# Performance work log

Hardware: AMD Instinct MI355X
Metric: run time of the kernel (lower is better)

## Reference

```python
import jax, jax.numpy as jnp
import numpy as np

B, O, N = 8, 100, 4096
TOK_D, D, K, H = 2048, 256, 128, 8
DH = D // H
LN_EPS = 1e-5


def _ln(x, g, b):
    m = x.mean(-1, keepdims=True)
    v = ((x - m) ** 2).mean(-1, keepdims=True)
    return (x - m) * jax.lax.rsqrt(v + LN_EPS) * g + b


def setup_inputs() -> dict:
    key = jax.random.key(0)
    ks = jax.random.split(key, 16)
    s = 0.02
    return {
        "activation": jax.random.uniform(ks[0], (B, O, N), jnp.float32),
        "tokens": jax.random.normal(ks[1], (B, N, TOK_D), jnp.float32),
        "W_tok": jax.random.normal(ks[2], (TOK_D, D), jnp.float32) * s,
        "b_tok": jnp.zeros((D,), jnp.float32),
        "g_tn": jnp.ones((D,), jnp.float32),
        "bt_tn": jnp.zeros((D,), jnp.float32),
        "pool_query": jax.random.normal(ks[3], (D,), jnp.float32) * s,
        "Wq": jax.random.normal(ks[4], (D, D), jnp.float32) * s,
        "bq": jnp.zeros((D,), jnp.float32),
        "Wk": jax.random.normal(ks[5], (D, D), jnp.float32) * s,
        "bk": jnp.zeros((D,), jnp.float32),
        "Wv": jax.random.normal(ks[6], (D, D), jnp.float32) * s,
        "bv": jnp.zeros((D,), jnp.float32),
        "Wo": jax.random.normal(ks[7], (D, D), jnp.float32) * s,
        "bo": jnp.zeros((D,), jnp.float32),
        "g_pn": jnp.ones((D,), jnp.float32),
        "bt_pn": jnp.zeros((D,), jnp.float32),
        "g_on": jnp.ones((D,), jnp.float32),
        "bt_on": jnp.zeros((D,), jnp.float32),
    }


def reference(activation, tokens, W_tok, b_tok, g_tn, bt_tn, pool_query,
              Wq, bq, Wk, bk, Wv, bv, Wo, bo, g_pn, bt_pn, g_on, bt_on):
    # project + norm the shared token pool: [B, N, D]
    tp = _ln(tokens @ W_tok + b_tok, g_tn, bt_tn)

    # weighted-average branch
    w = activation / jnp.clip(activation.sum(-1, keepdims=True), 1e-8)
    weighted_avg = jnp.einsum('bon,bnd->bod', w, tp)

    # top-k attention branch
    _, topk_idx = jax.lax.top_k(activation, K)            # [B, O, K]
    topk_tokens = jax.vmap(lambda t, i: t[i])(tp, topk_idx)  # [B, O, K, D]

    # MultiheadAttention with a single shared query vector (q_len = 1)
    q = (pool_query @ Wq + bq).reshape(H, DH)             # [H, DH]
    kp = (topk_tokens @ Wk + bk).reshape(B, O, K, H, DH)
    vp = (topk_tokens @ Wv + bv).reshape(B, O, K, H, DH)
    scores = jnp.einsum('hd,bokhd->bohk', q, kp) / np.sqrt(DH).astype(np.float32)
    attn = jax.nn.softmax(scores, axis=-1)                # [B, O, H, K]
    pooled = jnp.einsum('bohk,bokhd->bohd', attn, vp).reshape(B, O, D)
    pooled = _ln(pooled @ Wo + bo, g_pn, bt_pn)

    return _ln(weighted_avg + pooled, g_on, bt_on)
```

## Files before the change

### kernel.cpp

```cpp
#include <hip/hip_runtime.h>
#include <hip/hip_bf16.h>

#define DEVI static __device__ __forceinline__

typedef __attribute__((ext_vector_type(8))) short short8;
typedef __attribute__((ext_vector_type(4))) float f32x4;

#define B_   8
#define O_   100
#define N_   4096
#define TOKD 2048
#define D_   256
#define K_   128
#define H_   8
#define M_   (B_*N_)

DEVI unsigned short f2bf(float f) {
    unsigned u = __float_as_uint(f);
    u = (u + 0x7FFFu + ((u >> 16) & 1u)) >> 16;
    return (unsigned short)u;
}
DEVI float bf2f(unsigned v) { return __uint_as_float(v << 16); }

DEVI unsigned pkbf(float lo, float hi) {
    unsigned r;
    asm("v_cvt_pk_bf16_f32 %0, %1, %2" : "=v"(r) : "v"(lo), "v"(hi));
    return r;
}
DEVI void gload16(const void* g, void* l) {
    __builtin_amdgcn_global_load_lds((const __attribute__((address_space(1))) void*)g,
                                     (__attribute__((address_space(3))) void*)l, 16, 0, 0);
}

__global__ __launch_bounds__(256) void k_prep(const float* __restrict__ W,
                                              unsigned short* __restrict__ wtb,
                                              const float* __restrict__ pq,
                                              const float* __restrict__ Wq,
                                              const float* __restrict__ bqv,
                                              const float* __restrict__ Wk,
                                              const float* __restrict__ bkv,
                                              float* __restrict__ qW,
                                              float* __restrict__ qb) {
    const int t = threadIdx.x;
    if (blockIdx.x < 2048) {
        int idx = blockIdx.x * 256 + t;
        int k = idx >> 8, n = idx & 255;
        wtb[n * TOKD + k] = f2bf(W[idx]);
        return;
    }
    __shared__ float qpart[8][32];
    __shared__ float qhl[32];
    const int h = blockIdx.x - 2048;
    const int col = h * 32 + (t & 31), sl = t >> 5;
    float s = 0.f;
    #pragma unroll
    for (int e = 0; e < 32; ++e) s += pq[sl * 32 + e] * Wq[(sl * 32 + e) * D_ + col];
    qpart[sl][t & 31] = s;
    __syncthreads();
    if (t < 32) {
        float u = bqv[h * 32 + t];
        #pragma unroll
        for (int s8 = 0; s8 < 8; ++s8) u += qpart[s8][t];
        qhl[t] = u;
    }
    __syncthreads();
    float u = 0.f;
    #pragma unroll
    for (int dd = 0; dd < 32; ++dd) u += qhl[dd] * Wk[t * D_ + h * 32 + dd];
    qW[h * D_ + t] = u;
    if (t == 0) {
        float z = 0.f;
        for (int dd = 0; dd < 32; ++dd) z += qhl[dd] * bkv[h * 32 + dd];
        qb[h] = z;
    }
}

__global__ __launch_bounds__(512, 2) void k_gemm1(const float* __restrict__ A,
                                                  const unsigned short* __restrict__ Bt,
                                                  const float* __restrict__ btok,
                                                  const float* __restrict__ g,
                                                  const float* __restrict__ bt,
                                                  unsigned short* __restrict__ tp) {
    __shared__ __align__(16) char smem[98304];
    const int t = threadIdx.x;
    const int bm = blockIdx.x;
    const int lane = t & 63, w = t >> 6;
    const int wm = w >> 2, wn = w & 3;
    const int lr = lane >> 4, lc = lane & 15;

    const int arow = t >> 2;
    const int acb = (t & 3) * 32;
    const float* agp = A + (size_t)(bm * 128 + arow) * TOKD + (t & 3) * 16;
    const int aw0 = arow * 128 + (acb ^ ((arow & 7) << 4));
    const int aw1 = arow * 128 + ((acb + 16) ^ ((arow & 7) << 4));
    const unsigned short* bg = Bt + (size_t)(t >> 3) * TOKD
                        + (((((t & 7) << 4)) ^ (((t >> 3) & 7) << 4)) >> 1);
    char* bldsw = smem + 32768 + (t >> 6) * 1024;

    f32x4 acc[4][4] = {};
    const int NT = TOKD / 64;
    float4 a0, a1, a2, a3;

    a0 = *(const float4*)(agp);     a1 = *(const float4*)(agp + 4);
    a2 = *(const float4*)(agp + 8); a3 = *(const float4*)(agp + 12);
    #pragma unroll
    for (int c = 0; c < 4; ++c) gload16(bg + (size_t)c * 64 * TOKD, bldsw + c * 8192);
    {
        uint4 w0, w1;
        w0.x = pkbf(a0.x, a0.y); w0.y = pkbf(a0.z, a0.w);
        w0.z = pkbf(a1.x, a1.y); w0.w = pkbf(a1.z, a1.w);
        w1.x = pkbf(a2.x, a2.y); w1.y = pkbf(a2.z, a2.w);
        w1.z = pkbf(a3.x, a3.y); w1.w = pkbf(a3.z, a3.w);
        *(uint4*)(smem + aw0) = w0; *(uint4*)(smem + aw1) = w1;
    }
    a0 = *(const float4*)(agp + 64);  a1 = *(const float4*)(agp + 68);
    a2 = *(const float4*)(agp + 72);  a3 = *(const float4*)(agp + 76);
    asm volatile("s_waitcnt vmcnt(4) lgkmcnt(0)" ::: "memory");
    __builtin_amdgcn_s_barrier();

    int cur = 0;
    for (int kt = 0; kt < NT; ++kt) {
        const int nxt = cur ^ 1;
        if (kt + 1 < NT) {
            const unsigned short* bn = bg + (size_t)(kt + 1) * 64;
            #pragma unroll
            for (int c = 0; c < 4; ++c)
                gload16(bn + (size_t)c * 64 * TOKD, bldsw + nxt * 32768 + c * 8192);
        }
        const char* Ab = smem + cur * 16384;
        const char* Bb = smem + 32768 + cur * 32768;
        #pragma unroll
        for (int kk = 0; kk < 2; ++kk) {
            short8 afr[4], bfr[4];
            #pragma unroll
            for (int mi = 0; mi < 4; ++mi) {
                int row = wm * 64 + mi * 16 + lc;
                afr[mi] = *(const short8*)(Ab + row * 128 + ((kk * 64 + lr * 16) ^ ((row & 7) << 4)));
            }
            #pragma unroll
            for (int ni = 0; ni < 4; ++ni) {
                int n = wn * 64 + ni * 16 + lc;
                bfr[ni] = *(const short8*)(Bb + n * 128 + ((kk * 64 + lr * 16) ^ ((n & 7) << 4)));
            }
            __builtin_amdgcn_s_setprio(1);
            #pragma unroll
            for (int mi = 0; mi < 4; ++mi)
                #pragma unroll
                for (int ni = 0; ni < 4; ++ni)
                    acc[mi][ni] = __builtin_amdgcn_mfma_f32_16x16x32_bf16(afr[mi], bfr[ni], acc[mi][ni], 0, 0, 0);
            __builtin_amdgcn_s_setprio(0);
        }
        if (kt + 1 < NT) {
            char* Anw = smem + nxt * 16384;
            uint4 w0, w1;
            w0.x = pkbf(a0.x, a0.y); w0.y = pkbf(a0.z, a0.w);
            w0.z = pkbf(a1.x, a1.y); w0.w = pkbf(a1.z, a1.w);
            w1.x = pkbf(a2.x, a2.y); w1.y = pkbf(a2.z, a2.w);
            w1.z = pkbf(a3.x, a3.y); w1.w = pkbf(a3.z, a3.w);
            *(uint4*)(Anw + aw0) = w0; *(uint4*)(Anw + aw1) = w1;
            if (kt + 2 < NT) {
                const float* ap = agp + (size_t)(kt + 2) * 64;
                a0 = *(const float4*)(ap);     a1 = *(const float4*)(ap + 4);
                a2 = *(const float4*)(ap + 8); a3 = *(const float4*)(ap + 12);
                asm volatile("s_waitcnt vmcnt(4) lgkmcnt(0)" ::: "memory");
            } else {
                asm volatile("s_waitcnt vmcnt(0) lgkmcnt(0)" ::: "memory");
            }
            __builtin_amdgcn_s_barrier();
            cur = nxt;
        }
    }
    __syncthreads();

    float* ep = (float*)smem;
    const int col0 = lane * 4;
    float4 b4 = *(const float4*)(btok + col0);
    float4 g4 = *(const float4*)(g + col0);
    float4 t4 = *(const float4*)(bt + col0);
    #pragma unroll
    for (int chunk = 0; chunk < 2; ++chunk) {
        if (wm == chunk) {
            #pragma unroll
            for (int mi = 0; mi < 4; ++mi)
                #pragma unroll
                for (int ni = 0; ni < 4; ++ni)
                    #pragma unroll
                    for (int r = 0; r < 4; ++r)
                        ep[(mi * 16 + lr * 4 + r) * 260 + wn * 64 + ni * 16 + lc] = acc[mi][ni][r];
        }
        __syncthreads();
        #pragma unroll
        for (int rr = 0; rr < 8; ++rr) {
            int row = w * 8 + rr;
            float4 x4 = *(const float4*)(ep + row * 260 + col0);
            float x0 = x4.x + b4.x, x1 = x4.y + b4.y, x2 = x4.z + b4.z, x3 = x4.w + b4.w;
            float s = x0 + x1 + x2 + x3;
            float q = x0*x0 + x1*x1 + x2*x2 + x3*x3;
            #pragma unroll
            for (int m = 1; m < 64; m <<= 1) { s += __shfl_xor(s, m); q += __shfl_xor(q, m); }
            float mean = s * (1.f/256.f);
            float var = q * (1.f/256.f) - mean * mean;
            float rs = rsqrtf(var + 1e-5f);
            ushort4 o;
            o.x = f2bf((x0-mean)*rs*g4.x + t4.x);
            o.y = f2bf((x1-mean)*rs*g4.y + t4.y);
            o.z = f2bf((x2-mean)*rs*g4.z + t4.z);
            o.w = f2bf((x3-mean)*rs*g4.w + t4.w);
            *(ushort4*)(tp + (size_t)(bm * 128 + chunk * 64 + row) * D_ + col0) = o;
        }
        __syncthreads();
    }
}

__global__ __launch_bounds__(256) void k_topk(const float* __restrict__ act,
                                              int* __restrict__ oidx,
                                              float* __restrict__ asum) {
    __shared__ float redf[4];
    __shared__ int redi[4];
    __shared__ int cnts[2];
    __shared__ int eql[4096];
    const int t = threadIdx.x, lane = t & 63, wid = t >> 6;
    const int blk = blockIdx.x;
    const float* rp = act + (size_t)blk * N_;
    unsigned v[16];
    float fs = 0.f;
    #pragma unroll
    for (int i = 0; i < 16; ++i) {
        float f = rp[t + i * 256];
        v[i] = __float_as_uint(f);
        fs += f;
    }
    if (t == 0) { cnts[0] = 0; cnts[1] = 0; }
    #pragma unroll
    for (int m = 1; m < 64; m <<= 1) fs += __shfl_xor(fs, m);
    if (!lane) redf[wid] = fs;
    __syncthreads();
    if (t == 0) asum[blk] = fmaxf(redf[0] + redf[1] + redf[2] + redf[3], 1e-8f);

    unsigned thr = 0u;
    for (int bit = 31; bit >= 0; --bit) {
        unsigned cand = thr | (1u << bit);
        int c = 0;
        #pragma unroll
        for (int i = 0; i < 16; ++i) c += (v[i] >= cand) ? 1 : 0;
        #pragma unroll
        for (int m = 1; m < 64; m <<= 1) c += __shfl_xor(c, m);
        __syncthreads();
        if (!lane) redi[wid] = c;
        __syncthreads();
        int tot = redi[0] + redi[1] + redi[2] + redi[3];
        if (tot >= K_) thr = cand;
    }
    #pragma unroll
    for (int i = 0; i < 16; ++i) {
        unsigned x = v[i];
        if (x > thr) {
            int p = atomicAdd(&cnts[0], 1);
            oidx[blk * K_ + p] = t + i * 256;
        } else if (x == thr) {
            int p = atomicAdd(&cnts[1], 1);
            eql[p] = t + i * 256;
        }
    }
    __syncthreads();
    const int gc = cnts[0], E = cnts[1], m = K_ - gc;
    int last = -1;
    for (int slot = 0; slot < m; ++slot) {
        int best = 0x7FFFFFFF;
        for (int i = t; i < E; i += 256) {
            int e = eql[i];
            if (e > last && e < best) best = e;
        }
        #pragma unroll
        for (int mm = 1; mm < 64; mm <<= 1) best = min(best, __shfl_xor(best, mm));
        __syncthreads();
        if (!lane) redi[wid] = best;
        __syncthreads();
        best = min(min(redi[0], redi[1]), min(redi[2], redi[3]));
        if (t == 0) oidx[blk * K_ + gc + slot] = best;
        last = best;
    }
}

__global__ __launch_bounds__(256) void k_wavg(const float* __restrict__ act,
                                              const unsigned short* __restrict__ tp,
                                              float* __restrict__ partial) {
    const int kc = blockIdx.x;
    const int b = blockIdx.y;
    const int d = threadIdx.x;
    const unsigned short* tpb = tp + ((size_t)b * N_ + kc * 128) * D_ + d;
    const float* actb = act + (size_t)b * O_ * N_ + kc * 128;
    float* pout = partial + ((size_t)(b * 32 + kc) * O_) * D_ + d;
    for (int oci = 0; oci < 2; ++oci) {
        const int oc = blockIdx.z * 2 + oci;
        float acc[10] = {};
        for (int q = 0; q < 32; ++q) {
            float t0 = bf2f(tpb[(q * 4 + 0) * D_]);
            float t1 = bf2f(tpb[(q * 4 + 1) * D_]);
            float t2 = bf2f(tpb[(q * 4 + 2) * D_]);
            float t3 = bf2f(tpb[(q * 4 + 3) * D_]);
            #pragma unroll
            for (int oj = 0; oj < 10; ++oj) {
                float4 a4 = *(const float4*)(actb + (size_t)(oc * 10 + oj) * N_ + q * 4);
                acc[oj] += a4.x * t0 + a4.y * t1 + a4.z * t2 + a4.w * t3;
            }
        }
        #pragma unroll
        for (int oj = 0; oj < 10; ++oj)
            pout[(size_t)(oc * 10 + oj) * D_] = acc[oj];
    }
}

DEVI int swz(int j, int chunk) { return j * 512 + ((chunk ^ (j & 31)) << 4); }

__global__ __launch_bounds__(256) void k_attn(
    const unsigned short* __restrict__ tp, const int* __restrict__ oidx,
    const float* __restrict__ qW, const float* __restrict__ qbv,
    const float* __restrict__ Wv, const float* __restrict__ bv,
    const float* __restrict__ Wo, const float* __restrict__ bo,
    const float* __restrict__ g_pn, const float* __restrict__ bt_pn,
    const float* __restrict__ g_on, const float* __restrict__ bt_on,
    const float* __restrict__ partial, const float* __restrict__ asum,
    float* __restrict__ outp)
{
    __shared__ uint4 tgU[4096];
    __shared__ float sc[H_ * K_];
    __shared__ float ul[H_ * D_];
    __shared__ float pool_lds[D_];
    __shared__ float redf[8];
    __shared__ int idxl[K_];
    char* tg = (char*)tgU;

    const int t = threadIdx.x, lane = t & 63, wid = t >> 6;
    const int blk = blockIdx.x;
    const int b = blk / O_;
    const int o = blk - b * O_;

    if (t < K_) idxl[t] = oidx[blk * K_ + t];
    __syncthreads();

    #pragma unroll
    for (int it = 0; it < 16; ++it) {
        int c = t + it * 256;
        int j = c >> 5, ch = c & 31;
        uint4 v = *(const uint4*)(tp + ((size_t)(b * N_ + idxl[j])) * D_ + ch * 8);
        *(uint4*)(tg + swz(j, ch)) = v;
    }
    __syncthreads();

    {
        const int j = t & 127, hq = t >> 7;
        const float* q0 = qW + hq * 4 * D_;
        float s0 = 0.f, s1 = 0.f, s2 = 0.f, s3 = 0.f;
        #pragma unroll 4
        for (int e8 = 0; e8 < 32; ++e8) {
            uint4 tv = *(const uint4*)(tg + swz(j, e8));
            float f0 = bf2f(tv.x & 0xffffu), f1 = bf2f(tv.x >> 16);
            float f2 = bf2f(tv.y & 0xffffu), f3 = bf2f(tv.y >> 16);
            float f4 = bf2f(tv.z & 0xffffu), f5 = bf2f(tv.z >> 16);
            float f6 = bf2f(tv.w & 0xffffu), f7 = bf2f(tv.w >> 16);
            const float* qa = q0 + e8 * 8;
            const float* qbp = qa + D_;
            const float* qc = qa + 2 * D_;
            const float* qd = qa + 3 * D_;
            s0 += f0*qa[0]+f1*qa[1]+f2*qa[2]+f3*qa[3]+f4*qa[4]+f5*qa[5]+f6*qa[6]+f7*qa[7];
            s1 += f0*qbp[0]+f1*qbp[1]+f2*qbp[2]+f3*qbp[3]+f4*qbp[4]+f5*qbp[5]+f6*qbp[6]+f7*qbp[7];
            s2 += f0*qc[0]+f1*qc[1]+f2*qc[2]+f3*qc[3]+f4*qc[4]+f5*qc[5]+f6*qc[6]+f7*qc[7];
            s3 += f0*qd[0]+f1*qd[1]+f2*qd[2]+f3*qd[3]+f4*qd[4]+f5*qd[5]+f6*qd[6]+f7*qd[7];
        }
        const float sca = 0.1767766952966369f;
        sc[(hq * 4 + 0) * K_ + j] = (s0 + qbv[hq * 4 + 0]) * sca;
        sc[(hq * 4 + 1) * K_ + j] = (s1 + qbv[hq * 4 + 1]) * sca;
        sc[(hq * 4 + 2) * K_ + j] = (s2 + qbv[hq * 4 + 2]) * sca;
        sc[(hq * 4 + 3) * K_ + j] = (s3 + qbv[hq * 4 + 3]) * sca;
    }
    __syncthreads();

    #pragma unroll
    for (int hh = 0; hh < 2; ++hh) {
        int h = wid * 2 + hh;
        float v0 = sc[h * K_ + lane], v1 = sc[h * K_ + 64 + lane];
        float mx = fmaxf(v0, v1);
        #pragma unroll
        for (int m = 1; m < 64; m <<= 1) mx = fmaxf(mx, __shfl_xor(mx, m));
        float e0 = __expf(v0 - mx), e1 = __expf(v1 - mx);
        float ss = e0 + e1;
        #pragma unroll
        for (int m = 1; m < 64; m <<= 1) ss += __shfl_xor(ss, m);
        float inv = 1.0f / ss;
        sc[h * K_ + lane] = e0 * inv;
        sc[h * K_ + 64 + lane] = e1 * inv;
    }
    __syncthreads();

    {
        const int h = t >> 5, eg = t & 31;
        float a8[8] = {};
        #pragma unroll 2
        for (int jb = 0; jb < 32; ++jb) {
            f32x4 p4 = *(const f32x4*)(sc + h * K_ + jb * 4);
            #pragma unroll
            for (int ji = 0; ji < 4; ++ji) {
                int j = jb * 4 + ji;
                uint4 tv = *(const uint4*)(tg + swz(j, eg));
                float pw = p4[ji];
                a8[0] += pw * bf2f(tv.x & 0xffffu); a8[1] += pw * bf2f(tv.x >> 16);
                a8[2] += pw * bf2f(tv.y & 0xffffu); a8[3] += pw * bf2f(tv.y >> 16);
                a8[4] += pw * bf2f(tv.z & 0xffffu); a8[5] += pw * bf2f(tv.z >> 16);
                a8[6] += pw * bf2f(tv.w & 0xffffu); a8[7] += pw * bf2f(tv.w >> 16);
            }
        }
        #pragma unroll
        for (int i = 0; i < 8; ++i) ul[h * D_ + eg * 8 + i] = a8[i];
    }
    __syncthreads();

    {
        int h = t >> 5;
        const float* up = ul + h * D_;
        float p = bv[t];
        for (int e = 0; e < D_; ++e) p += up[e] * Wv[e * D_ + t];
        pool_lds[t] = p;
    }
    __syncthreads();
    float po = bo[t];
    for (int e = 0; e < D_; ++e) po += pool_lds[e] * Wo[e * D_ + t];

    float s1 = po, q1 = po * po;
    #pragma unroll
    for (int m = 1; m < 64; m <<= 1) { s1 += __shfl_xor(s1, m); q1 += __shfl_xor(q1, m); }
    if (!lane) { redf[wid] = s1; redf[4 + wid] = q1; }
    __syncthreads();
    s1 = redf[0] + redf[1] + redf[2] + redf[3];
    q1 = redf[4] + redf[5] + redf[6] + redf[7];
    float mean = s1 * (1.f/256.f);
    float var = q1 * (1.f/256.f) - mean * mean;
    float rs = rsqrtf(var + 1e-5f);
    float pl = (po - mean) * rs * g_pn[t] + bt_pn[t];
    __syncthreads();

    float wa = 0.f;
    const float* pp = partial + ((size_t)(b * 32) * O_ + o) * D_ + t;
    #pragma unroll 8
    for (int kc = 0; kc < 32; ++kc) wa += pp[(size_t)kc * O_ * D_];
    float x = wa / asum[blk] + pl;
    float s2 = x, q2 = x * x;
    #pragma unroll
    for (int m = 1; m < 64; m <<= 1) { s2 += __shfl_xor(s2, m); q2 += __shfl_xor(q2, m); }
    if (!lane) { redf[wid] = s2; redf[4 + wid] = q2; }
    __syncthreads();
    s2 = redf[0] + redf[1] + redf[2] + redf[3];
    q2 = redf[4] + redf[5] + redf[6] + redf[7];
    float mean2 = s2 * (1.f/256.f);
    float var2 = q2 * (1.f/256.f) - mean2 * mean2;
    float rs2 = rsqrtf(var2 + 1e-5f);
    outp[(size_t)blk * D_ + t] = (x - mean2) * rs2 * g_on[t] + bt_on[t];
}

extern "C" void kernel_launch(void* const* d_in, const int* in_sizes, int n_in,
                              void* d_out, int out_size, void* d_ws, size_t ws_size,
                              hipStream_t stream) {
    const float* act    = (const float*)d_in[0];
    const float* tokens = (const float*)d_in[1];
    const float* W_tok  = (const float*)d_in[2];
    const float* b_tok  = (const float*)d_in[3];
    const float* g_tn   = (const float*)d_in[4];
    const float* bt_tn  = (const float*)d_in[5];
    const float* pq     = (const float*)d_in[6];
    const float* Wq     = (const float*)d_in[7];
    const float* bq     = (const float*)d_in[8];
    const float* Wk     = (const float*)d_in[9];
    const float* bk     = (const float*)d_in[10];
    const float* Wv     = (const float*)d_in[11];
    const float* bv     = (const float*)d_in[12];
    const float* Wo     = (const float*)d_in[13];
    const float* bo     = (const float*)d_in[14];
    const float* g_pn   = (const float*)d_in[15];
    const float* bt_pn  = (const float*)d_in[16];
    const float* g_on   = (const float*)d_in[17];
    const float* bt_on  = (const float*)d_in[18];

    char* ws = (char*)d_ws;
    unsigned short* wtb   = (unsigned short*)ws;
    unsigned short* tp    = (unsigned short*)(ws + 1048576);
    int*   tidx = (int*)(ws + 17825792);
    float* asum = (float*)(ws + 18235392);
    float* part = (float*)(ws + 18238592);
    float* qW   = (float*)(ws + 44452992);
    float* qb   = (float*)(ws + 44461184);

    k_prep<<<2056, 256, 0, stream>>>(W_tok, wtb, pq, Wq, bq, Wk, bk, qW, qb);
    k_gemm1<<<M_ / 128, 512, 0, stream>>>(tokens, wtb, b_tok, g_tn, bt_tn, tp);
    k_topk<<<B_ * O_, 256, 0, stream>>>(act, tidx, asum);
    k_wavg<<<dim3(32, 8, 5), 256, 0, stream>>>(act, tp, part);
    k_attn<<<B_ * O_, 256, 0, stream>>>(tp, tidx, qW, qb, Wv, bv, Wo, bo,
                                        g_pn, bt_pn, g_on, bt_on, part, asum,
                                        (float*)d_out);
}
```

Measured before the change: 225.2 us.

## Replace bitwise radix top-k with histogram select fused into prep kernel

```diff
diff --git a/kernel.cpp b/kernel.cpp
--- a/kernel.cpp
+++ b/kernel.cpp
@@ -32,46 +32,154 @@
                                      (__attribute__((address_space(3))) void*)l, 16, 0, 0);
 }
 
-__global__ __launch_bounds__(256) void k_prep(const float* __restrict__ W,
-                                              unsigned short* __restrict__ wtb,
-                                              const float* __restrict__ pq,
-                                              const float* __restrict__ Wq,
-                                              const float* __restrict__ bqv,
-                                              const float* __restrict__ Wk,
-                                              const float* __restrict__ bkv,
-                                              float* __restrict__ qW,
-                                              float* __restrict__ qb) {
-    const int t = threadIdx.x;
-    if (blockIdx.x < 2048) {
-        int idx = blockIdx.x * 256 + t;
-        int k = idx >> 8, n = idx & 255;
-        wtb[n * TOKD + k] = f2bf(W[idx]);
+__global__ __launch_bounds__(256) void k_pre(const float* __restrict__ act,
+                                             int* __restrict__ oidx,
+                                             float* __restrict__ asum,
+                                             const float* __restrict__ W,
+                                             unsigned short* __restrict__ wtb,
+                                             const float* __restrict__ pq,
+                                             const float* __restrict__ Wq,
+                                             const float* __restrict__ bqv,
+                                             const float* __restrict__ Wk,
+                                             const float* __restrict__ bkv,
+                                             float* __restrict__ qW,
+                                             float* __restrict__ qb) {
+    __shared__ __align__(16) char smem[50304];
+    const int t = threadIdx.x, lane = t & 63, wid = t >> 6;
+
+    if (blockIdx.x >= 800) {
+        const int bx = blockIdx.x - 800;
+        if (bx < 2048) {
+            int idx = bx * 256 + t;
+            int k = idx >> 8, n = idx & 255;
+            wtb[n * TOKD + k] = f2bf(W[idx]);
+            return;
+        }
+        float (*qpart)[32] = (float(*)[32])smem;
+        float* qhl = (float*)(smem + 1024);
+        const int h = bx - 2048;
+        const int col = h * 32 + (t & 31), sl = t >> 5;
+        float s = 0.f;
+        #pragma unroll
+        for (int e = 0; e < 32; ++e) s += pq[sl * 32 + e] * Wq[(sl * 32 + e) * D_ + col];
+        qpart[sl][t & 31] = s;
+        __syncthreads();
+        if (t < 32) {
+            float u = bqv[h * 32 + t];
+            #pragma unroll
+            for (int s8 = 0; s8 < 8; ++s8) u += qpart[s8][t];
+            qhl[t] = u;
+        }
+        __syncthreads();
+        float u = 0.f;
+        #pragma unroll
+        for (int dd = 0; dd < 32; ++dd) u += qhl[dd] * Wk[t * D_ + h * 32 + dd];
+        qW[h * D_ + t] = u;
+        if (t == 0) {
+            float z = 0.f;
+            for (int dd = 0; dd < 32; ++dd) z += qhl[dd] * bkv[h * 32 + dd];
+            qb[h] = z;
+        }
         return;
     }
-    __shared__ float qpart[8][32];
-    __shared__ float qhl[32];
-    const int h = blockIdx.x - 2048;
-    const int col = h * 32 + (t & 31), sl = t >> 5;
-    float s = 0.f;
-    #pragma unroll
-    for (int e = 0; e < 32; ++e) s += pq[sl * 32 + e] * Wq[(sl * 32 + e) * D_ + col];
-    qpart[sl][t & 31] = s;
-    __syncthreads();
-    if (t < 32) {
-        float u = bqv[h * 32 + t];
-        #pragma unroll
-        for (int s8 = 0; s8 < 8; ++s8) u += qpart[s8][t];
-        qhl[t] = u;
-    }
-    __syncthreads();
-    float u = 0.f;
-    #pragma unroll
-    for (int dd = 0; dd < 32; ++dd) u += qhl[dd] * Wk[t * D_ + h * 32 + dd];
-    qW[h * D_ + t] = u;
-    if (t == 0) {
-        float z = 0.f;
-        for (int dd = 0; dd < 32; ++dd) z += qhl[dd] * bkv[h * 32 + dd];
-        qb[h] = z;
+
+    int* hist = (int*)smem;
+    unsigned long long* cand = (unsigned long long*)(smem + 16384);
+    int* csum = (int*)(smem + 49152);
+    int* sb   = (int*)(smem + 50192);
+    int* cnts = (int*)(smem + 50200);
+    float* redf = (float*)(smem + 50208);
+    unsigned long long* redu = (unsigned long long*)(smem + 50224);
+
+    const int blk = blockIdx.x;
+    const float* rp = act + (size_t)blk * N_;
+    float fv[16]; unsigned vb[16]; int bins[16];
+    float fs = 0.f;
+    #pragma unroll
+    for (int i = 0; i < 16; ++i) {
+        float f = rp[t + i * 256];
+        fv[i] = f; vb[i] = __float_as_uint(f);
+        fs += f;
+    }
+    #pragma unroll
+    for (int i = 0; i < 16; ++i) hist[t + i * 256] = 0;
+    if (t == 0) { cnts[0] = 0; cnts[1] = 0; }
+    #pragma unroll
+    for (int m = 1; m < 64; m <<= 1) fs += __shfl_xor(fs, m);
+    if (!lane) redf[wid] = fs;
+    __syncthreads();
+    if (t == 0) asum[blk] = fmaxf(redf[0] + redf[1] + redf[2] + redf[3], 1e-8f);
+
+    #pragma unroll
+    for (int i = 0; i < 16; ++i) {
+        float f = fv[i];
+        int b = (f >= 1.0f) ? 4095 : ((f > 0.f) ? (int)(f * 4096.f) : 0);
+        bins[i] = b;
+        atomicAdd(&hist[b], 1);
+    }
+    __syncthreads();
+
+    int cs = 0;
+    #pragma unroll
+    for (int i = 0; i < 16; ++i) cs += hist[t * 16 + i];
+    int v = cs;
+    #pragma unroll
+    for (int off = 1; off < 64; off <<= 1) {
+        int o = __shfl_down(v, off);
+        if (lane + off < 64) v += o;
+    }
+    if (!lane) csum[256 + wid] = v;
+    __syncthreads();
+    int stot = 0;
+    for (int w2 = wid + 1; w2 < 4; ++w2) stot += csum[256 + w2];
+    int suff = v + stot;
+    csum[t] = suff;
+    __syncthreads();
+    int nxtc = (t < 255) ? csum[t + 1] : 0;
+    if (suff >= K_ && nxtc < K_) {
+        int run = nxtc, bstar = t * 16;
+        for (int bi = 15; bi >= 0; --bi) {
+            run += hist[t * 16 + bi];
+            if (run >= K_) { bstar = t * 16 + bi; break; }
+        }
+        sb[0] = bstar;
+    }
+    __syncthreads();
+    const int bstar = sb[0];
+
+    #pragma unroll
+    for (int i = 0; i < 16; ++i) {
+        if (bins[i] > bstar) {
+            int p = atomicAdd(&cnts[0], 1);
+            oidx[blk * K_ + p] = t + i * 256;
+        } else if (bins[i] == bstar) {
+            int p = atomicAdd(&cnts[1], 1);
+            cand[p] = ((unsigned long long)vb[i] << 16) | (unsigned)(4095 - (t + i * 256));
+        }
+    }
+    __syncthreads();
+    const int g = cnts[0], E = cnts[1], m = K_ - g;
+    unsigned long long last = ~0ull;
+    for (int slot = 0; slot < m; ++slot) {
+        unsigned long long best = 0;
+        for (int i = t; i < E; i += 256) {
+            unsigned long long e = cand[i];
+            if (e < last && e > best) best = e;
+        }
+        #pragma unroll
+        for (int mm = 1; mm < 64; mm <<= 1) {
+            unsigned long long o = __shfl_xor(best, mm);
+            if (o > best) best = o;
+        }
+        if (!lane) redu[wid] = best;
+        __syncthreads();
+        best = redu[0];
+        if (redu[1] > best) best = redu[1];
+        if (redu[2] > best) best = redu[2];
+        if (redu[3] > best) best = redu[3];
+        if (t == 0) oidx[blk * K_ + g + slot] = 4095 - (int)(best & 0xFFFFull);
+        last = best;
+        __syncthreads();
     }
 }
 
@@ -212,76 +320,6 @@
     }
 }
 
-__global__ __launch_bounds__(256) void k_topk(const float* __restrict__ act,
-                                              int* __restrict__ oidx,
-                                              float* __restrict__ asum) {
-    __shared__ float redf[4];
-    __shared__ int redi[4];
-    __shared__ int cnts[2];
-    __shared__ int eql[4096];
-    const int t = threadIdx.x, lane = t & 63, wid = t >> 6;
-    const int blk = blockIdx.x;
-    const float* rp = act + (size_t)blk * N_;
-    unsigned v[16];
-    float fs = 0.f;
-    #pragma unroll
-    for (int i = 0; i < 16; ++i) {
-        float f = rp[t + i * 256];
-        v[i] = __float_as_uint(f);
-        fs += f;
-    }
-    if (t == 0) { cnts[0] = 0; cnts[1] = 0; }
-    #pragma unroll
-    for (int m = 1; m < 64; m <<= 1) fs += __shfl_xor(fs, m);
-    if (!lane) redf[wid] = fs;
-    __syncthreads();
-    if (t == 0) asum[blk] = fmaxf(redf[0] + redf[1] + redf[2] + redf[3], 1e-8f);
-
-    unsigned thr = 0u;
-    for (int bit = 31; bit >= 0; --bit) {
-        unsigned cand = thr | (1u << bit);
-        int c = 0;
-        #pragma unroll
-        for (int i = 0; i < 16; ++i) c += (v[i] >= cand) ? 1 : 0;
-        #pragma unroll
-        for (int m = 1; m < 64; m <<= 1) c += __shfl_xor(c, m);
-        __syncthreads();
-        if (!lane) redi[wid] = c;
-        __syncthreads();
-        int tot = redi[0] + redi[1] + redi[2] + redi[3];
-        if (tot >= K_) thr = cand;
-    }
-    #pragma unroll
-    for (int i = 0; i < 16; ++i) {
-        unsigned x = v[i];
-        if (x > thr) {
-            int p = atomicAdd(&cnts[0], 1);
-            oidx[blk * K_ + p] = t + i * 256;
-        } else if (x == thr) {
-            int p = atomicAdd(&cnts[1], 1);
-            eql[p] = t + i * 256;
-        }
-    }
-    __syncthreads();
-    const int gc = cnts[0], E = cnts[1], m = K_ - gc;
-    int last = -1;
-    for (int slot = 0; slot < m; ++slot) {
-        int best = 0x7FFFFFFF;
-        for (int i = t; i < E; i += 256) {
-            int e = eql[i];
-            if (e > last && e < best) best = e;
-        }
-        #pragma unroll
-        for (int mm = 1; mm < 64; mm <<= 1) best = min(best, __shfl_xor(best, mm));
-        __syncthreads();
-        if (!lane) redi[wid] = best;
-        __syncthreads();
-        best = min(min(redi[0], redi[1]), min(redi[2], redi[3]));
-        if (t == 0) oidx[blk * K_ + gc + slot] = best;
-        last = best;
-    }
-}
-
 __global__ __launch_bounds__(256) void k_wavg(const float* __restrict__ act,
                                               const unsigned short* __restrict__ tp,
                                               float* __restrict__ partial) {
@@ -294,6 +332,7 @@
     for (int oci = 0; oci < 2; ++oci) {
         const int oc = blockIdx.z * 2 + oci;
         float acc[10] = {};
+        #pragma unroll 2
         for (int q = 0; q < 32; ++q) {
             float t0 = bf2f(tpb[(q * 4 + 0) * D_]);
             float t1 = bf2f(tpb[(q * 4 + 1) * D_]);
@@ -419,11 +458,13 @@
         int h = t >> 5;
         const float* up = ul + h * D_;
         float p = bv[t];
+        #pragma unroll 8
         for (int e = 0; e < D_; ++e) p += up[e] * Wv[e * D_ + t];
         pool_lds[t] = p;
     }
     __syncthreads();
     float po = bo[t];
+    #pragma unroll 8
     for (int e = 0; e < D_; ++e) po += pool_lds[e] * Wo[e * D_ + t];
 
     float s1 = po, q1 = po * po;
@@ -489,9 +530,9 @@
     float* qW   = (float*)(ws + 44452992);
     float* qb   = (float*)(ws + 44461184);
 
-    k_prep<<<2056, 256, 0, stream>>>(W_tok, wtb, pq, Wq, bq, Wk, bk, qW, qb);
+    k_pre<<<2856, 256, 0, stream>>>(act, tidx, asum, W_tok, wtb,
+                                    pq, Wq, bq, Wk, bk, qW, qb);
     k_gemm1<<<M_ / 128, 512, 0, stream>>>(tokens, wtb, b_tok, g_tn, bt_tn, tp);
-    k_topk<<<B_ * O_, 256, 0, stream>>>(act, tidx, asum);
     k_wavg<<<dim3(32, 8, 5), 256, 0, stream>>>(act, tp, part);
     k_attn<<<B_ * O_, 256, 0, stream>>>(tp, tidx, qW, qb, Wv, bv, Wo, bo,
                                         g_pn, bt_pn, g_on, bt_on, part, asum,
```

Result: no change. 226.1 us (+0.4%).
